# Performance work log

Hardware: AMD Instinct MI355X
Metric: run time of the kernel (lower is better)

Reference implementation:

```python
import jax, jax.numpy as jnp
import numpy as np

F = 256      # n_features
N = 128      # n_nodes
B = 4096     # batch


def setup_inputs() -> dict:
    key = jax.random.key(0)
    ks = jax.random.split(key, 11)
    s = lambda *sh: 1.0 / np.sqrt(sh[-2]) if len(sh) >= 2 else 1.0
    x = jax.random.normal(ks[0], (B, F), dtype=jnp.float32)
    # Block-diagonal weights: [F, in, out] per stage; biases [F, out]
    w1 = jax.random.normal(ks[1], (F, 1, N), dtype=jnp.float32)
    b1 = jax.random.normal(ks[2], (F, N), dtype=jnp.float32) * 0.01
    w2 = jax.random.normal(ks[3], (F, N, N), dtype=jnp.float32) / np.sqrt(N)
    b2 = jax.random.normal(ks[4], (F, N), dtype=jnp.float32) * 0.01
    w3 = jax.random.normal(ks[5], (F, N, N), dtype=jnp.float32) / np.sqrt(N)
    b3 = jax.random.normal(ks[6], (F, N), dtype=jnp.float32) * 0.01
    w4 = jax.random.normal(ks[7], (F, N, 1), dtype=jnp.float32) / np.sqrt(N)
    b4 = jax.random.normal(ks[8], (F, 1), dtype=jnp.float32) * 0.01
    # Final linear: [F, 1] weight, [1] bias
    lr_w = jax.random.normal(ks[9], (F, 1), dtype=jnp.float32) / np.sqrt(F)
    lr_b = jax.random.normal(ks[10], (1,), dtype=jnp.float32) * 0.01
    return {"x": x, "w1": w1, "b1": b1, "w2": w2, "b2": b2,
            "w3": w3, "b3": b3, "w4": w4, "b4": b4,
            "lr_w": lr_w, "lr_b": lr_b}


def reference(x, w1, b1, w2, b2, w3, b3, w4, b4, lr_w, lr_b):
    # Per-feature block-diagonal MLP chain with ReLU between stages.
    # x: [B, F] -> view each feature as a 1-dim input to its own subnet.
    h = x[:, :, None]                                   # [B, F, 1]
    h = jax.nn.relu(jnp.einsum('bfi,fio->bfo', h, w1) + b1)   # [B, F, N]
    h = jax.nn.relu(jnp.einsum('bfi,fio->bfo', h, w2) + b2)   # [B, F, N]
    h = jax.nn.relu(jnp.einsum('bfi,fio->bfo', h, w3) + b3)   # [B, F, N]
    h = jnp.einsum('bfi,fio->bfo', h, w4) + b4                # [B, F, 1]
    x_pre = h[:, :, 0]                                        # [B, F]
    return x_pre @ lr_w + lr_b                                # [B, 1]
```

## Files before the change

kernel.cpp:

```cpp
#include <hip/hip_runtime.h>
#include <hip/hip_bf16.h>

#define F_DIM 256
#define N_DIM 128
#define B_DIM 4096

typedef float f32x4v __attribute__((ext_vector_type(4)));
typedef float f32x16v __attribute__((ext_vector_type(16)));
typedef short s16x8 __attribute__((ext_vector_type(8)));
typedef unsigned int u32x4v __attribute__((ext_vector_type(4)));

__device__ __forceinline__ unsigned short f2bf(float f) {
  union { float f; unsigned u; } v; v.f = f;
  unsigned r = v.u + 0x7fffu + ((v.u >> 16) & 1u);
  return (unsigned short)(r >> 16);
}

__device__ __forceinline__ unsigned pk2(float a, float b) {
  union { __hip_bfloat16 h[2]; unsigned u; } v;
  v.h[0] = __float2bfloat16(a);
  v.h[1] = __float2bfloat16(b);
  return v.u;
}

__device__ __forceinline__ void gload16(const void* g, void* l) {
  __builtin_amdgcn_global_load_lds(
      (const __attribute__((address_space(1))) unsigned int*)g,
      (__attribute__((address_space(3))) unsigned int*)l, 16, 0, 0);
}

__device__ __forceinline__ s16x8 frag1(unsigned d) {
  u32x4v v = {d, 0u, 0u, 0u};
  return __builtin_bit_cast(s16x8, v);
}

__device__ __forceinline__ void cvt_swap(f32x16v a, s16x8* f0, s16x8* f1) {
  unsigned P[8];
#pragma unroll
  for (int q = 0; q < 8; ++q)
    P[q] = pk2(fmaxf(a[2 * q], 0.f), fmaxf(a[2 * q + 1], 0.f));
  asm volatile("v_permlane32_swap_b32 %0, %1" : "+v"(P[0]), "+v"(P[2]));
  asm volatile("v_permlane32_swap_b32 %0, %1" : "+v"(P[1]), "+v"(P[3]));
  asm volatile("v_permlane32_swap_b32 %0, %1" : "+v"(P[4]), "+v"(P[6]));
  asm volatile("v_permlane32_swap_b32 %0, %1" : "+v"(P[5]), "+v"(P[7]));
  u32x4v lo = {P[0], P[1], P[2], P[3]};
  u32x4v hh = {P[4], P[5], P[6], P[7]};
  *f0 = __builtin_bit_cast(s16x8, lo);
  *f1 = __builtin_bit_cast(s16x8, hh);
}

__global__ void prep_w(const float* __restrict__ w2, const float* __restrict__ w3,
                       unsigned int* __restrict__ wTs) {
  __shared__ float tile[128 * 130];
  int m = blockIdx.x;
  const float* src = (m < 256) ? (w2 + (size_t)m * 16384)
                               : (w3 + (size_t)(m - 256) * 16384);
  int t = threadIdx.x;
  for (int k = 0; k < 64; ++k) {
    int idx = k * 256 + t;
    int i = idx >> 7, o = idx & 127;
    tile[o * 130 + i] = src[idx];
  }
  __syncthreads();
  unsigned int* dst = wTs + (size_t)m * 8192;
  for (int k = 0; k < 32; ++k) {
    int idx = k * 256 + t;
    int o = idx >> 6, i2 = idx & 63;
    unsigned pk = (unsigned)f2bf(tile[o * 130 + 2 * i2]) |
                  ((unsigned)f2bf(tile[o * 130 + 2 * i2 + 1]) << 16);
    dst[(o * 64 + i2) ^ ((o & 15) << 2)] = pk;
  }
}

__global__ void prep_x(const float* __restrict__ x, float* __restrict__ xT) {
  __shared__ float tile[64][65];
  int btile = blockIdx.x & 63;
  int ftile = blockIdx.x >> 6;
  int t = threadIdx.x;
  for (int k = 0; k < 16; ++k) {
    int idx = k * 256 + t;
    int r = idx >> 6, c = idx & 63;
    tile[r][c] = x[(size_t)(btile * 64 + r) * F_DIM + ftile * 64 + c];
  }
  __syncthreads();
  for (int k = 0; k < 16; ++k) {
    int idx = k * 256 + t;
    int fr = idx >> 6, br = idx & 63;
    xT[(size_t)(ftile * 64 + fr) * B_DIM + btile * 64 + br] = tile[br][fr];
  }
}

__global__ __launch_bounds__(512, 2) void mlp_chain(
    const float* __restrict__ xT, const float* __restrict__ w1,
    const float* __restrict__ b1, const float* __restrict__ b2,
    const float* __restrict__ b3, const float* __restrict__ w4,
    const float* __restrict__ b4, const unsigned int* __restrict__ wTs,
    float* __restrict__ xp) {
  __shared__ __align__(16) char Wb[2][128 * 256];
  __shared__ __align__(16) float w4l[N_DIM];

  const int f    = blockIdx.x >> 1;
  const int half = blockIdx.x & 1;
  const int t    = threadIdx.x;
  const int lane = t & 63, wid = t >> 6;
  const int c32  = lane & 31, hi = lane >> 5;

  {
    const char* s2 = (const char*)(wTs + (size_t)f * 8192);
    const char* s3 = (const char*)(wTs + (size_t)(256 + f) * 8192);
#pragma unroll
    for (int c = 0; c < 4; ++c) {
      int off = (wid * 4 + c) * 1024;
      gload16(s2 + off + lane * 16, &Wb[0][off]);
    }
#pragma unroll
    for (int c = 0; c < 4; ++c) {
      int off = (wid * 4 + c) * 1024;
      gload16(s3 + off + lane * 16, &Wb[1][off]);
    }
    if (t < 32) *(f32x4v*)&w4l[t * 4] = *(const f32x4v*)&w4[f * N_DIM + t * 4];
  }

  unsigned a1d[4], a2d[4], a3d[4];
#pragma unroll
  for (int it = 0; it < 4; ++it) {
    int i = it * 32 + c32;
    float w1v = w1[f * N_DIM + i], b1v = b1[f * N_DIM + i];
    float b2v = b2[f * N_DIM + i], b3v = b3[f * N_DIM + i];
    a1d[it] = hi ? 0u : pk2(w1v, b1v);
    a2d[it] = hi ? 0u : pk2(0.f, b2v);
    a3d[it] = hi ? 0u : pk2(0.f, b3v);
  }
  const float b4f = b4[f];
  const float* xcol = xT + (size_t)f * B_DIM + half * 2048;
  float* xprow = xp + (size_t)f * B_DIM + half * 2048;

  const int wbase = c32 * 256 + (((lane & 15) ^ hi) << 4);

  __syncthreads();

  const f32x16v zero = {0.f, 0.f, 0.f, 0.f, 0.f, 0.f, 0.f, 0.f,
                        0.f, 0.f, 0.f, 0.f, 0.f, 0.f, 0.f, 0.f};

  float xv = xcol[wid * 32 + c32];
#pragma unroll 1
  for (int itb = 0; itb < 8; ++itb) {
    const int bb = itb * 256 + wid * 32;
    s16x8 Bx = frag1(hi ? 0u : pk2(xv, 1.0f));
    float xv_n = (itb < 7) ? xcol[bb + 256 + c32] : 0.f;

    s16x8 h1f[8];
#pragma unroll
    for (int it = 0; it < 4; ++it) {
      f32x16v h = __builtin_amdgcn_mfma_f32_32x32x16_bf16(frag1(a1d[it]), Bx,
                                                          zero, 0, 0, 0);
      cvt_swap(h, &h1f[2 * it], &h1f[2 * it + 1]);
    }

    f32x16v acc3[4];
#pragma unroll
    for (int nt = 0; nt < 4; ++nt) {
      f32x16v a2 = __builtin_amdgcn_mfma_f32_32x32x16_bf16(frag1(a2d[nt]), Bx,
                                                           zero, 0, 0, 0);
#pragma unroll
      for (int m = 0; m < 8; ++m) {
        s16x8 af = *(const s16x8*)(&Wb[0][0] + nt * 8192 + (wbase ^ (m << 5)));
        a2 = __builtin_amdgcn_mfma_f32_32x32x16_bf16(af, h1f[m], a2, 0, 0, 0);
      }
      s16x8 h2a, h2b;
      cvt_swap(a2, &h2a, &h2b);
#pragma unroll
      for (int n3 = 0; n3 < 4; ++n3) {
        if (nt == 0)
          acc3[n3] = __builtin_amdgcn_mfma_f32_32x32x16_bf16(frag1(a3d[n3]), Bx,
                                                             zero, 0, 0, 0);
        s16x8 af0 = *(const s16x8*)(&Wb[1][0] + n3 * 8192 +
                                    (wbase ^ ((2 * nt) << 5)));
        acc3[n3] = __builtin_amdgcn_mfma_f32_32x32x16_bf16(af0, h2a, acc3[n3],
                                                           0, 0, 0);
        s16x8 af1 = *(const s16x8*)(&Wb[1][0] + n3 * 8192 +
                                    (wbase ^ ((2 * nt + 1) << 5)));
        acc3[n3] = __builtin_amdgcn_mfma_f32_32x32x16_bf16(af1, h2b, acc3[n3],
                                                           0, 0, 0);
      }
    }

    float p = 0.f;
#pragma unroll
    for (int n3 = 0; n3 < 4; ++n3)
#pragma unroll
      for (int q = 0; q < 4; ++q) {
        f32x4v wv = *(const f32x4v*)&w4l[n3 * 32 + q * 8 + hi * 4];
#pragma unroll
        for (int i = 0; i < 4; ++i)
          p = fmaf(fmaxf(acc3[n3][4 * q + i], 0.f), wv[i], p);
      }
    p += __shfl_xor(p, 32, 64);
    if (hi == 0) xprow[bb + c32] = p + b4f;
    xv = xv_n;
  }
}

__global__ void final_reduce(const float* __restrict__ xp,
                             const float* __restrict__ lr_w,
                             const float* __restrict__ lr_b,
                             float* __restrict__ out) {
  __shared__ float lw[F_DIM];
  __shared__ float part[4][64];
  int t = threadIdx.x;
  if (t < F_DIM) lw[t] = lr_w[t];
  __syncthreads();
  int q = t >> 6, bl = t & 63;
  int b = blockIdx.x * 64 + bl;
  float acc = 0.f;
#pragma unroll 8
  for (int j = 0; j < 64; ++j) {
    int ff = q * 64 + j;
    acc += xp[(size_t)ff * B_DIM + b] * lw[ff];
  }
  part[q][bl] = acc;
  __syncthreads();
  if (q == 0)
    out[b] = part[0][bl] + part[1][bl] + part[2][bl] + part[3][bl] + lr_b[0];
}

extern "C" void kernel_launch(void* const* d_in, const int* in_sizes, int n_in,
                              void* d_out, int out_size, void* d_ws, size_t ws_size,
                              hipStream_t stream) {
  (void)in_sizes; (void)n_in; (void)out_size; (void)ws_size;
  const float* x    = (const float*)d_in[0];
  const float* w1   = (const float*)d_in[1];
  const float* b1   = (const float*)d_in[2];
  const float* w2   = (const float*)d_in[3];
  const float* b2   = (const float*)d_in[4];
  const float* w3   = (const float*)d_in[5];
  const float* b3   = (const float*)d_in[6];
  const float* w4   = (const float*)d_in[7];
  const float* b4   = (const float*)d_in[8];
  const float* lr_w = (const float*)d_in[9];
  const float* lr_b = (const float*)d_in[10];
  float* out = (float*)d_out;

  char* ws = (char*)d_ws;
  unsigned int* wTs = (unsigned int*)ws;
  float* xT = (float*)(ws + (16u << 20));
  float* xp = (float*)(ws + (16u << 20) + (4u << 20));

  prep_w<<<512, 256, 0, stream>>>(w2, w3, wTs);
  prep_x<<<256, 256, 0, stream>>>(x, xT);
  mlp_chain<<<512, 512, 0, stream>>>(xT, w1, b1, b2, b3, w4, b4, wTs, xp);
  final_reduce<<<64, 256, 0, stream>>>(xp, lr_w, lr_b, out);
}
```

Before: 105.7 us.

## Process two batch tiles per wave, reusing weight fragments across both

Each wave now handles two 32-row batch tiles at once, so every LDS weight fragment read feeds two MFMAs instead of one. The block shrinks to 4 waves and the grid grows to 1024 blocks (four per feature, each covering 1024 batch rows). Layer 3 is restructured to run after all of layer 2, which keeps the full h2 fragments in registers. The permlane asm loses its volatile qualifier so the compiler can schedule it freely. The cost is higher register pressure from the doubled accumulators and fragments, and each block still loads the full 64KB of weights into LDS for a quarter of the batch.

```diff
diff --git a/kernel.cpp b/kernel.cpp
--- a/kernel.cpp
+++ b/kernel.cpp
@@ -39,10 +39,10 @@
 #pragma unroll
   for (int q = 0; q < 8; ++q)
     P[q] = pk2(fmaxf(a[2 * q], 0.f), fmaxf(a[2 * q + 1], 0.f));
-  asm volatile("v_permlane32_swap_b32 %0, %1" : "+v"(P[0]), "+v"(P[2]));
-  asm volatile("v_permlane32_swap_b32 %0, %1" : "+v"(P[1]), "+v"(P[3]));
-  asm volatile("v_permlane32_swap_b32 %0, %1" : "+v"(P[4]), "+v"(P[6]));
-  asm volatile("v_permlane32_swap_b32 %0, %1" : "+v"(P[5]), "+v"(P[7]));
+  asm("v_permlane32_swap_b32 %0, %1" : "+v"(P[0]), "+v"(P[2]));
+  asm("v_permlane32_swap_b32 %0, %1" : "+v"(P[1]), "+v"(P[3]));
+  asm("v_permlane32_swap_b32 %0, %1" : "+v"(P[4]), "+v"(P[6]));
+  asm("v_permlane32_swap_b32 %0, %1" : "+v"(P[5]), "+v"(P[7]));
   u32x4v lo = {P[0], P[1], P[2], P[3]};
   u32x4v hh = {P[4], P[5], P[6], P[7]};
   *f0 = __builtin_bit_cast(s16x8, lo);
@@ -90,7 +90,7 @@
   }
 }
 
-__global__ __launch_bounds__(512, 2) void mlp_chain(
+__global__ __launch_bounds__(256, 2) void mlp_chain(
     const float* __restrict__ xT, const float* __restrict__ w1,
     const float* __restrict__ b1, const float* __restrict__ b2,
     const float* __restrict__ b3, const float* __restrict__ w4,
@@ -99,23 +99,23 @@
   __shared__ __align__(16) char Wb[2][128 * 256];
   __shared__ __align__(16) float w4l[N_DIM];
 
-  const int f    = blockIdx.x >> 1;
-  const int half = blockIdx.x & 1;
-  const int t    = threadIdx.x;
+  const int f  = blockIdx.x >> 2;
+  const int qt = blockIdx.x & 3;
+  const int t  = threadIdx.x;
   const int lane = t & 63, wid = t >> 6;
-  const int c32  = lane & 31, hi = lane >> 5;
+  const int c32 = lane & 31, hi = lane >> 5;
 
   {
     const char* s2 = (const char*)(wTs + (size_t)f * 8192);
     const char* s3 = (const char*)(wTs + (size_t)(256 + f) * 8192);
 #pragma unroll
-    for (int c = 0; c < 4; ++c) {
-      int off = (wid * 4 + c) * 1024;
+    for (int c = 0; c < 8; ++c) {
+      int off = (wid * 8 + c) * 1024;
       gload16(s2 + off + lane * 16, &Wb[0][off]);
     }
 #pragma unroll
-    for (int c = 0; c < 4; ++c) {
-      int off = (wid * 4 + c) * 1024;
+    for (int c = 0; c < 8; ++c) {
+      int off = (wid * 8 + c) * 1024;
       gload16(s3 + off + lane * 16, &Wb[1][off]);
     }
     if (t < 32) *(f32x4v*)&w4l[t * 4] = *(const f32x4v*)&w4[f * N_DIM + t * 4];
@@ -132,8 +132,8 @@
     a3d[it] = hi ? 0u : pk2(0.f, b3v);
   }
   const float b4f = b4[f];
-  const float* xcol = xT + (size_t)f * B_DIM + half * 2048;
-  float* xprow = xp + (size_t)f * B_DIM + half * 2048;
+  const float* xcol = xT + (size_t)f * B_DIM + qt * 1024;
+  float* xprow = xp + (size_t)f * B_DIM + qt * 1024;
 
   const int wbase = c32 * 256 + (((lane & 15) ^ hi) << 4);
 
@@ -142,62 +142,75 @@
   const f32x16v zero = {0.f, 0.f, 0.f, 0.f, 0.f, 0.f, 0.f, 0.f,
                         0.f, 0.f, 0.f, 0.f, 0.f, 0.f, 0.f, 0.f};
 
-  float xv = xcol[wid * 32 + c32];
+  float xvA = xcol[wid * 64 + c32];
+  float xvB = xcol[wid * 64 + 32 + c32];
 #pragma unroll 1
-  for (int itb = 0; itb < 8; ++itb) {
-    const int bb = itb * 256 + wid * 32;
-    s16x8 Bx = frag1(hi ? 0u : pk2(xv, 1.0f));
-    float xv_n = (itb < 7) ? xcol[bb + 256 + c32] : 0.f;
-
-    s16x8 h1f[8];
+  for (int itb = 0; itb < 4; ++itb) {
+    const int bb = itb * 256 + wid * 64;
+    s16x8 BxA = frag1(hi ? 0u : pk2(xvA, 1.0f));
+    s16x8 BxB = frag1(hi ? 0u : pk2(xvB, 1.0f));
+    float xvA_n = (itb < 3) ? xcol[bb + 256 + c32] : 0.f;
+    float xvB_n = (itb < 3) ? xcol[bb + 256 + 32 + c32] : 0.f;
+
+    s16x8 h1A[8], h1B[8];
 #pragma unroll
     for (int it = 0; it < 4; ++it) {
-      f32x16v h = __builtin_amdgcn_mfma_f32_32x32x16_bf16(frag1(a1d[it]), Bx,
-                                                          zero, 0, 0, 0);
-      cvt_swap(h, &h1f[2 * it], &h1f[2 * it + 1]);
-    }
-
-    f32x16v acc3[4];
+      f32x16v hA = __builtin_amdgcn_mfma_f32_32x32x16_bf16(frag1(a1d[it]), BxA,
+                                                           zero, 0, 0, 0);
+      cvt_swap(hA, &h1A[2 * it], &h1A[2 * it + 1]);
+      f32x16v hB = __builtin_amdgcn_mfma_f32_32x32x16_bf16(frag1(a1d[it]), BxB,
+                                                           zero, 0, 0, 0);
+      cvt_swap(hB, &h1B[2 * it], &h1B[2 * it + 1]);
+    }
+
+    s16x8 h2A[8], h2B[8];
 #pragma unroll
     for (int nt = 0; nt < 4; ++nt) {
-      f32x16v a2 = __builtin_amdgcn_mfma_f32_32x32x16_bf16(frag1(a2d[nt]), Bx,
-                                                           zero, 0, 0, 0);
+      f32x16v a2A = __builtin_amdgcn_mfma_f32_32x32x16_bf16(frag1(a2d[nt]), BxA,
+                                                            zero, 0, 0, 0);
+      f32x16v a2B = __builtin_amdgcn_mfma_f32_32x32x16_bf16(frag1(a2d[nt]), BxB,
+                                                            zero, 0, 0, 0);
 #pragma unroll
       for (int m = 0; m < 8; ++m) {
         s16x8 af = *(const s16x8*)(&Wb[0][0] + nt * 8192 + (wbase ^ (m << 5)));
-        a2 = __builtin_amdgcn_mfma_f32_32x32x16_bf16(af, h1f[m], a2, 0, 0, 0);
+        a2A = __builtin_amdgcn_mfma_f32_32x32x16_bf16(af, h1A[m], a2A, 0, 0, 0);
+        a2B = __builtin_amdgcn_mfma_f32_32x32x16_bf16(af, h1B[m], a2B, 0, 0, 0);
       }
-      s16x8 h2a, h2b;
-      cvt_swap(a2, &h2a, &h2b);
-#pragma unroll
-      for (int n3 = 0; n3 < 4; ++n3) {
-        if (nt == 0)
-          acc3[n3] = __builtin_amdgcn_mfma_f32_32x32x16_bf16(frag1(a3d[n3]), Bx,
-                                                             zero, 0, 0, 0);
-        s16x8 af0 = *(const s16x8*)(&Wb[1][0] + n3 * 8192 +
-                                    (wbase ^ ((2 * nt) << 5)));
-        acc3[n3] = __builtin_amdgcn_mfma_f32_32x32x16_bf16(af0, h2a, acc3[n3],
-                                                           0, 0, 0);
-        s16x8 af1 = *(const s16x8*)(&Wb[1][0] + n3 * 8192 +
-                                    (wbase ^ ((2 * nt + 1) << 5)));
-        acc3[n3] = __builtin_amdgcn_mfma_f32_32x32x16_bf16(af1, h2b, acc3[n3],
-                                                           0, 0, 0);
+      cvt_swap(a2A, &h2A[2 * nt], &h2A[2 * nt + 1]);
+      cvt_swap(a2B, &h2B[2 * nt], &h2B[2 * nt + 1]);
+    }
+
+    float pA = 0.f, pB = 0.f;
+#pragma unroll
+    for (int n3 = 0; n3 < 4; ++n3) {
+      f32x16v a3A = __builtin_amdgcn_mfma_f32_32x32x16_bf16(frag1(a3d[n3]), BxA,
+                                                            zero, 0, 0, 0);
+      f32x16v a3B = __builtin_amdgcn_mfma_f32_32x32x16_bf16(frag1(a3d[n3]), BxB,
+                                                            zero, 0, 0, 0);
+#pragma unroll
+      for (int k = 0; k < 8; ++k) {
+        s16x8 af = *(const s16x8*)(&Wb[1][0] + n3 * 8192 + (wbase ^ (k << 5)));
+        a3A = __builtin_amdgcn_mfma_f32_32x32x16_bf16(af, h2A[k], a3A, 0, 0, 0);
+        a3B = __builtin_amdgcn_mfma_f32_32x32x16_bf16(af, h2B[k], a3B, 0, 0, 0);
       }
-    }
-
-    float p = 0.f;
-#pragma unroll
-    for (int n3 = 0; n3 < 4; ++n3)
 #pragma unroll
       for (int q = 0; q < 4; ++q) {
         f32x4v wv = *(const f32x4v*)&w4l[n3 * 32 + q * 8 + hi * 4];
 #pragma unroll
-        for (int i = 0; i < 4; ++i)
-          p = fmaf(fmaxf(acc3[n3][4 * q + i], 0.f), wv[i], p);
+        for (int i = 0; i < 4; ++i) {
+          pA = fmaf(fmaxf(a3A[4 * q + i], 0.f), wv[i], pA);
+          pB = fmaf(fmaxf(a3B[4 * q + i], 0.f), wv[i], pB);
+        }
       }
-    p += __shfl_xor(p, 32, 64);
-    if (hi == 0) xprow[bb + c32] = p + b4f;
-    xv = xv_n;
+    }
+    pA += __shfl_xor(pA, 32, 64);
+    pB += __shfl_xor(pB, 32, 64);
+    if (hi == 0) {
+      xprow[bb + c32]      = pA + b4f;
+      xprow[bb + 32 + c32] = pB + b4f;
+    }
+    xvA = xvA_n;
+    xvB = xvB_n;
   }
 }
 
@@ -248,6 +261,6 @@
 
   prep_w<<<512, 256, 0, stream>>>(w2, w3, wTs);
   prep_x<<<256, 256, 0, stream>>>(x, xT);
-  mlp_chain<<<512, 512, 0, stream>>>(xT, w1, b1, b2, b3, w4, b4, wTs, xp);
+  mlp_chain<<<1024, 256, 0, stream>>>(xT, w1, b1, b2, b3, w4, b4, wTs, xp);
   final_reduce<<<64, 256, 0, stream>>>(xp, lr_w, lr_b, out);
 }
```

Result: faster. 103.3 us (-2.3%).

## Restructure MLP chain into paired MFMA streams with packed ReLU and permuted weight layout

Applied to the files above, without the earlier changes.

Replaces the interleaved layer-2/layer-3 accumulation with two separate phases. Each phase runs two independent MFMA accumulator chains together, under raised wave priority, to hide MFMA dependency latency. The permlane32 swaps are removed by permuting the bf16 weight layout in prep_w so the MFMA output maps directly to the next layer's B operand. ReLU is done after packing via v_pk_max_i16 on the bf16 pairs, and the final w4 dot uses packed float2 FMAs. LDS offsets are precomputed and pinned in registers, which adds register pressure and materialises all eight h2 fragments at once.

```diff
diff --git a/kernel.cpp b/kernel.cpp
--- a/kernel.cpp
+++ b/kernel.cpp
@@ -5,10 +5,13 @@
 #define N_DIM 128
 #define B_DIM 4096
 
+typedef float f32x2v __attribute__((ext_vector_type(2)));
 typedef float f32x4v __attribute__((ext_vector_type(4)));
 typedef float f32x16v __attribute__((ext_vector_type(16)));
 typedef short s16x8 __attribute__((ext_vector_type(8)));
 typedef unsigned int u32x4v __attribute__((ext_vector_type(4)));
+
+#define PIN(x) asm("" : "+v"(x))
 
 __device__ __forceinline__ unsigned short f2bf(float f) {
   union { float f; unsigned u; } v; v.f = f;
@@ -34,19 +37,21 @@
   return __builtin_bit_cast(s16x8, v);
 }
 
-__device__ __forceinline__ void cvt_swap(f32x16v a, s16x8* f0, s16x8* f1) {
+struct frag2 { s16x8 lo, hi; };
+
+__device__ __forceinline__ frag2 cvt2(f32x16v a) {
   unsigned P[8];
 #pragma unroll
-  for (int q = 0; q < 8; ++q)
-    P[q] = pk2(fmaxf(a[2 * q], 0.f), fmaxf(a[2 * q + 1], 0.f));
-  asm volatile("v_permlane32_swap_b32 %0, %1" : "+v"(P[0]), "+v"(P[2]));
-  asm volatile("v_permlane32_swap_b32 %0, %1" : "+v"(P[1]), "+v"(P[3]));
-  asm volatile("v_permlane32_swap_b32 %0, %1" : "+v"(P[4]), "+v"(P[6]));
-  asm volatile("v_permlane32_swap_b32 %0, %1" : "+v"(P[5]), "+v"(P[7]));
+  for (int q = 0; q < 8; ++q) {
+    unsigned pk = pk2(a[2 * q], a[2 * q + 1]);
+    asm("v_pk_max_i16 %0, %1, 0" : "=v"(P[q]) : "v"(pk));
+  }
   u32x4v lo = {P[0], P[1], P[2], P[3]};
   u32x4v hh = {P[4], P[5], P[6], P[7]};
-  *f0 = __builtin_bit_cast(s16x8, lo);
-  *f1 = __builtin_bit_cast(s16x8, hh);
+  frag2 r;
+  r.lo = __builtin_bit_cast(s16x8, lo);
+  r.hi = __builtin_bit_cast(s16x8, hh);
+  return r;
 }
 
 __global__ void prep_w(const float* __restrict__ w2, const float* __restrict__ w3,
@@ -68,7 +73,9 @@
     int o = idx >> 6, i2 = idx & 63;
     unsigned pk = (unsigned)f2bf(tile[o * 130 + 2 * i2]) |
                   ((unsigned)f2bf(tile[o * 130 + 2 * i2 + 1]) << 16);
-    dst[(o * 64 + i2) ^ ((o & 15) << 2)] = pk;
+    int w = i2 & 7;
+    int i2p = (i2 & ~7) + ((w >> 1) & 1) * 4 + (w & 1) + (((w >> 2) & 1) << 1);
+    dst[(o * 64) + (i2p ^ ((o & 15) << 2))] = pk;
   }
 }
 
@@ -103,7 +110,7 @@
   const int half = blockIdx.x & 1;
   const int t    = threadIdx.x;
   const int lane = t & 63, wid = t >> 6;
-  const int c32  = lane & 31, hi = lane >> 5;
+  const int c32 = lane & 31, hi = lane >> 5;
 
   {
     const char* s2 = (const char*)(wTs + (size_t)f * 8192);
@@ -136,11 +143,16 @@
   float* xprow = xp + (size_t)f * B_DIM + half * 2048;
 
   const int wbase = c32 * 256 + (((lane & 15) ^ hi) << 4);
+  int va[8];
+#pragma unroll
+  for (int m = 0; m < 8; ++m) { va[m] = wbase ^ (m << 5); PIN(va[m]); }
+  const char* wb = &Wb[0][0];
 
   __syncthreads();
 
   const f32x16v zero = {0.f, 0.f, 0.f, 0.f, 0.f, 0.f, 0.f, 0.f,
                         0.f, 0.f, 0.f, 0.f, 0.f, 0.f, 0.f, 0.f};
+  const f32x2v zz = {0.f, 0.f};
 
   float xv = xcol[wid * 32 + c32];
 #pragma unroll 1
@@ -149,52 +161,76 @@
     s16x8 Bx = frag1(hi ? 0u : pk2(xv, 1.0f));
     float xv_n = (itb < 7) ? xcol[bb + 256 + c32] : 0.f;
 
-    s16x8 h1f[8];
+    s16x8 h1[8];
 #pragma unroll
     for (int it = 0; it < 4; ++it) {
       f32x16v h = __builtin_amdgcn_mfma_f32_32x32x16_bf16(frag1(a1d[it]), Bx,
                                                           zero, 0, 0, 0);
-      cvt_swap(h, &h1f[2 * it], &h1f[2 * it + 1]);
-    }
-
-    f32x16v acc3[4];
-#pragma unroll
-    for (int nt = 0; nt < 4; ++nt) {
-      f32x16v a2 = __builtin_amdgcn_mfma_f32_32x32x16_bf16(frag1(a2d[nt]), Bx,
-                                                           zero, 0, 0, 0);
+      frag2 r = cvt2(h);
+      h1[2 * it] = r.lo;  h1[2 * it + 1] = r.hi;
+      PIN(h1[2 * it]);  PIN(h1[2 * it + 1]);
+    }
+
+    s16x8 h2[8];
+#pragma unroll
+    for (int ntp = 0; ntp < 2; ++ntp) {
+      const int nt0 = 2 * ntp, nt1 = nt0 + 1;
+      f32x16v u0 = __builtin_amdgcn_mfma_f32_32x32x16_bf16(frag1(a2d[nt0]), Bx,
+                                                           zero, 0, 0, 0);
+      f32x16v u1 = __builtin_amdgcn_mfma_f32_32x32x16_bf16(frag1(a2d[nt1]), Bx,
+                                                           zero, 0, 0, 0);
+      __builtin_amdgcn_s_setprio(1);
 #pragma unroll
       for (int m = 0; m < 8; ++m) {
-        s16x8 af = *(const s16x8*)(&Wb[0][0] + nt * 8192 + (wbase ^ (m << 5)));
-        a2 = __builtin_amdgcn_mfma_f32_32x32x16_bf16(af, h1f[m], a2, 0, 0, 0);
+        s16x8 af0 = *(const s16x8*)(wb + va[m] + nt0 * 8192);
+        s16x8 af1 = *(const s16x8*)(wb + va[m] + nt1 * 8192);
+        u0 = __builtin_amdgcn_mfma_f32_32x32x16_bf16(af0, h1[m], u0, 0, 0, 0);
+        u1 = __builtin_amdgcn_mfma_f32_32x32x16_bf16(af1, h1[m], u1, 0, 0, 0);
       }
-      s16x8 h2a, h2b;
-      cvt_swap(a2, &h2a, &h2b);
-#pragma unroll
-      for (int n3 = 0; n3 < 4; ++n3) {
-        if (nt == 0)
-          acc3[n3] = __builtin_amdgcn_mfma_f32_32x32x16_bf16(frag1(a3d[n3]), Bx,
-                                                             zero, 0, 0, 0);
-        s16x8 af0 = *(const s16x8*)(&Wb[1][0] + n3 * 8192 +
-                                    (wbase ^ ((2 * nt) << 5)));
-        acc3[n3] = __builtin_amdgcn_mfma_f32_32x32x16_bf16(af0, h2a, acc3[n3],
-                                                           0, 0, 0);
-        s16x8 af1 = *(const s16x8*)(&Wb[1][0] + n3 * 8192 +
-                                    (wbase ^ ((2 * nt + 1) << 5)));
-        acc3[n3] = __builtin_amdgcn_mfma_f32_32x32x16_bf16(af1, h2b, acc3[n3],
-                                                           0, 0, 0);
+      __builtin_amdgcn_s_setprio(0);
+      frag2 r0 = cvt2(u0);
+      h2[2 * nt0] = r0.lo;  h2[2 * nt0 + 1] = r0.hi;
+      PIN(h2[2 * nt0]);  PIN(h2[2 * nt0 + 1]);
+      frag2 r1 = cvt2(u1);
+      h2[2 * nt1] = r1.lo;  h2[2 * nt1 + 1] = r1.hi;
+      PIN(h2[2 * nt1]);  PIN(h2[2 * nt1 + 1]);
+    }
+
+    f32x2v p0 = zz, p1 = zz;
+#pragma unroll
+    for (int n3p = 0; n3p < 2; ++n3p) {
+      const int n30 = 2 * n3p, n31 = n30 + 1;
+      f32x16v v0 = __builtin_amdgcn_mfma_f32_32x32x16_bf16(frag1(a3d[n30]), Bx,
+                                                           zero, 0, 0, 0);
+      f32x16v v1 = __builtin_amdgcn_mfma_f32_32x32x16_bf16(frag1(a3d[n31]), Bx,
+                                                           zero, 0, 0, 0);
+      __builtin_amdgcn_s_setprio(1);
+#pragma unroll
+      for (int k = 0; k < 8; ++k) {
+        s16x8 af0 = *(const s16x8*)(wb + va[k] + 32768 + n30 * 8192);
+        s16x8 af1 = *(const s16x8*)(wb + va[k] + 32768 + n31 * 8192);
+        v0 = __builtin_amdgcn_mfma_f32_32x32x16_bf16(af0, h2[k], v0, 0, 0, 0);
+        v1 = __builtin_amdgcn_mfma_f32_32x32x16_bf16(af1, h2[k], v1, 0, 0, 0);
       }
-    }
-
-    float p = 0.f;
-#pragma unroll
-    for (int n3 = 0; n3 < 4; ++n3)
+      __builtin_amdgcn_s_setprio(0);
 #pragma unroll
       for (int q = 0; q < 4; ++q) {
-        f32x4v wv = *(const f32x4v*)&w4l[n3 * 32 + q * 8 + hi * 4];
-#pragma unroll
-        for (int i = 0; i < 4; ++i)
-          p = fmaf(fmaxf(acc3[n3][4 * q + i], 0.f), wv[i], p);
+        f32x2v w01_0 = *(const f32x2v*)&w4l[n30 * 32 + q * 8 + hi * 4];
+        f32x2v w23_0 = *(const f32x2v*)&w4l[n30 * 32 + q * 8 + hi * 4 + 2];
+        f32x2v w01_1 = *(const f32x2v*)&w4l[n31 * 32 + q * 8 + hi * 4];
+        f32x2v w23_1 = *(const f32x2v*)&w4l[n31 * 32 + q * 8 + hi * 4 + 2];
+        f32x2v r;
+        r[0] = fmaxf(v0[4 * q + 0], 0.f); r[1] = fmaxf(v0[4 * q + 1], 0.f);
+        p0 += r * w01_0;
+        r[0] = fmaxf(v0[4 * q + 2], 0.f); r[1] = fmaxf(v0[4 * q + 3], 0.f);
+        p1 += r * w23_0;
+        r[0] = fmaxf(v1[4 * q + 0], 0.f); r[1] = fmaxf(v1[4 * q + 1], 0.f);
+        p0 += r * w01_1;
+        r[0] = fmaxf(v1[4 * q + 2], 0.f); r[1] = fmaxf(v1[4 * q + 3], 0.f);
+        p1 += r * w23_1;
       }
+    }
+    float p = p0[0] + p0[1] + p1[0] + p1[1];
     p += __shfl_xor(p, 32, 64);
     if (hi == 0) xprow[bb + c32] = p + b4f;
     xv = xv_n;
```

Result: faster. 99.25 us (-6.1%).
